# Optimization experiments

Hardware: AMD Instinct MI355X
Metric: run time of the kernel (lower is better)

## Reference

```python
import jax, jax.numpy as jnp
import numpy as np

D_MODEL = 1024
NHEAD = 16
HEAD_DIM = D_MODEL // NHEAD
SF_THRESHOLD = 4.0
SF_LEVELS = 8
SF_STEP = SF_THRESHOLD / SF_LEVELS  # 0.5
EPS = 1e-6


def sfn(x):
    # Scale-and-Fire neuron: quantize activations to multiples of SF_STEP,
    # clipped to +/- num_levels, with straight-through estimator.
    q = jnp.clip(jnp.round(x / SF_STEP), -SF_LEVELS, SF_LEVELS) * SF_STEP
    return x + jax.lax.stop_gradient(q - x)


def qk_norm(x, g):
    # RMS-normalize over the head_dim (last axis) with learnable gain g [Dh].
    rms = jnp.sqrt(jnp.mean(x * x, axis=-1, keepdims=True) + EPS)
    return (x / rms) * g


def setup_inputs() -> dict:
    key = jax.random.key(0)
    ks = jax.random.split(key, 10)
    B, L, D = 2, 2048, D_MODEL
    s = 1.0 / np.sqrt(D)
    return {
        "x": jax.random.normal(ks[0], (B, L, D), dtype=jnp.float32),
        "Wq": jax.random.normal(ks[1], (D, D), dtype=jnp.float32) * s,
        "bq": jnp.zeros((D,), dtype=jnp.float32),
        "Wk": jax.random.normal(ks[2], (D, D), dtype=jnp.float32) * s,
        "bk": jnp.zeros((D,), dtype=jnp.float32),
        "Wv": jax.random.normal(ks[3], (D, D), dtype=jnp.float32) * s,
        "bv": jnp.zeros((D,), dtype=jnp.float32),
        "Wo": jax.random.normal(ks[4], (D, D), dtype=jnp.float32) * s,
        "bo": jnp.zeros((D,), dtype=jnp.float32),
        "gq": jnp.ones((HEAD_DIM,), dtype=jnp.float32),
        "gk": jnp.ones((HEAD_DIM,), dtype=jnp.float32),
    }


def reference(x, Wq, bq, Wk, bk, Wv, bv, Wo, bo, gq, gk):
    B, L, D = x.shape
    H, Dh = NHEAD, HEAD_DIM
    scale = Dh ** (-0.5)

    q = sfn(x @ Wq.T + bq)
    k = sfn(x @ Wk.T + bk)
    v = sfn(x @ Wv.T + bv)

    # [B, L, H, Dh] -> [B, H, L, Dh]
    q = q.reshape(B, L, H, Dh).transpose(0, 2, 1, 3)
    k = k.reshape(B, L, H, Dh).transpose(0, 2, 1, 3)
    v = v.reshape(B, L, H, Dh).transpose(0, 2, 1, 3)

    q = qk_norm(q, gq)
    k = qk_norm(k, gk)

    scores = jnp.einsum('bhqd,bhkd->bhqk', q, k) * scale
    probs = jax.nn.softmax(scores, axis=-1)  # dropout is identity (eval)
    out = jnp.einsum('bhqk,bhkd->bhqd', probs, v)
    out = out.transpose(0, 2, 1, 3).reshape(B, L, D)
    return out @ Wo.T + bo
```

## Files before the change

kernel.cpp:

```cpp
#include <hip/hip_runtime.h>
#include <math.h>


typedef __bf16 bf16;
typedef bf16 bf16x4 __attribute__((ext_vector_type(4)));
typedef bf16 bf16x8 __attribute__((ext_vector_type(8)));
typedef float f32x4 __attribute__((ext_vector_type(4)));

#define LOG2E 1.4426950408889634f
#define MFMA16 __builtin_amdgcn_mfma_f32_16x16x32_bf16
#define S_WAITV(N) asm volatile("s_waitcnt vmcnt(" #N ")" ::: "memory")

__device__ __forceinline__ void bar() {
  asm volatile("" ::: "memory");
  __builtin_amdgcn_s_barrier();
  asm volatile("" ::: "memory");
}

__device__ __forceinline__ float sfn_f(float x) {
  return fminf(fmaxf(rintf(x + x), -8.0f), 8.0f) * 0.5f;
}

__device__ __forceinline__ void gload16(const bf16* g, bf16* l) {
  __builtin_amdgcn_global_load_lds((const __attribute__((address_space(1))) void*)g,
                                   (__attribute__((address_space(3))) void*)l, 16, 0, 0);
}


__global__ __launch_bounds__(256) void prep_x_kernel(const float* __restrict__ x,
                                                     bf16* __restrict__ ax) {
  int idx = blockIdx.x * 256 + threadIdx.x;
  int m  = idx >> 8;
  int kc = (idx & 255) << 2;
  const float4 v = *(const float4*)(x + (size_t)m * 1024 + kc);
  bf16 h0 = (bf16)v.x, h1 = (bf16)v.y, h2 = (bf16)v.z, h3 = (bf16)v.w;
  bf16 l0 = (bf16)(v.x - (float)h0), l1 = (bf16)(v.y - (float)h1),
       l2 = (bf16)(v.z - (float)h2), l3 = (bf16)(v.w - (float)h3);
  bf16x4 hv = {h0, h1, h2, h3};
  bf16x4 lv = {l0, l1, l2, l3};
  bf16* p = ax + (size_t)m * 3072 + kc;
  *(bf16x4*)(p)        = hv;
  *(bf16x4*)(p + 1024) = lv;
  *(bf16x4*)(p + 2048) = hv;
}

__global__ __launch_bounds__(256) void prep_w_kernel(const float* __restrict__ Wq,
                                                     const float* __restrict__ Wk,
                                                     const float* __restrict__ Wv,
                                                     bf16* __restrict__ wc) {
  int idx = blockIdx.x * 256 + threadIdx.x;
  int mat = idx >> 18;
  int r   = idx & 262143;
  int n   = r >> 8;
  int kc  = (r & 255) << 2;
  const float* W = (mat == 0) ? Wq : ((mat == 1) ? Wk : Wv);
  const float4 v = *(const float4*)(W + (size_t)n * 1024 + kc);
  bf16 h0 = (bf16)v.x, h1 = (bf16)v.y, h2 = (bf16)v.z, h3 = (bf16)v.w;
  bf16 l0 = (bf16)(v.x - (float)h0), l1 = (bf16)(v.y - (float)h1),
       l2 = (bf16)(v.z - (float)h2), l3 = (bf16)(v.w - (float)h3);
  bf16x4 hv = {h0, h1, h2, h3};
  bf16x4 lv = {l0, l1, l2, l3};
  bf16* p = wc + (size_t)(mat * 1024 + n) * 3072 + kc;
  *(bf16x4*)(p)        = hv;
  *(bf16x4*)(p + 1024) = hv;
  *(bf16x4*)(p + 2048) = lv;
}

__global__ __launch_bounds__(256) void prep_wo_kernel(const float* __restrict__ Wo,
                                                      bf16* __restrict__ wob) {
  int idx = blockIdx.x * 256 + threadIdx.x;
  const float4 v = *(const float4*)(Wo + (size_t)idx * 4);
  bf16x4 hv = {(bf16)v.x, (bf16)v.y, (bf16)v.z, (bf16)v.w};
  *(bf16x4*)(wob + (size_t)idx * 4) = hv;
}


__global__ __launch_bounds__(512, 2) void gemm_qkv_kernel(
    const bf16* __restrict__ A, const bf16* __restrict__ Bm,
    const float* __restrict__ b0, const float* __restrict__ b1,
    const float* __restrict__ b2, const float* __restrict__ g0,
    const float* __restrict__ g1, bf16* __restrict__ qn, bf16* __restrict__ kn,
    bf16* __restrict__ vt) {
  constexpr int K = 3072, NT = 48;
  __shared__ bf16 lds[2][28672];
  const int tid  = threadIdx.x;
  const int wave = tid >> 6;
  const int lane = tid & 63;
  const int lm   = lane & 15;
  const int kg   = lane >> 4;
  const int lid     = blockIdx.x;
  const int logical = ((lid & 7) << 5) | (lid >> 3);
  const int m0 = (logical >> 4) << 8;
  const int n0 = (logical & 15) * 192;

  auto stageA = [&](int buf, int half, int kt) {
#pragma unroll
    for (int j = 0; j < 2; ++j) {
      const int c    = j * 512 + tid;
      const int row  = c >> 3;
      const int col8 = (c & 7) ^ (row & 7);
      gload16(A + (size_t)(m0 + half * 128 + row) * K + kt + col8 * 8,
              &lds[buf][half * 8192 + c * 8]);
    }
  };
  auto stageB = [&](int buf, int ch, int kt) {
    const int row  = tid >> 3;
    const int col8 = (tid & 7) ^ (row & 7);
    gload16(Bm + (size_t)(n0 + ch * 64 + row) * K + kt + col8 * 8,
            &lds[buf][16384 + ch * 4096 + tid * 8]);
  };

  const int sw    = lm & 7;
  const int arow  = (wave << 5) + lm;
  auto rdA = [&](int buf, int r, int kk) -> bf16x8 {
    const int row = arow + 16 * r;
    return *(const bf16x8*)&lds[buf][(row >> 7) * 8192 + (row & 127) * 64 +
                                     (((kk << 2) + kg) ^ sw) * 8];
  };
  auto rdB = [&](int buf, int c, int kk) -> bf16x8 {
    const int col = 16 * c + lm;
    return *(const bf16x8*)&lds[buf][16384 + (col >> 6) * 4096 + (col & 63) * 64 +
                                     (((kk << 2) + kg) ^ sw) * 8];
  };

  f32x4 acc[2][12] = {};

  stageA(0, 0, 0); stageA(0, 1, 0);
  stageB(0, 0, 0); stageB(0, 1, 0); stageB(0, 2, 0);
  stageA(1, 0, 64); stageA(1, 1, 64);
  S_WAITV(4);
  bar();

  for (int t = 0; t < NT; ++t) {
    const int cur = t & 1, nxt = cur ^ 1;
    const int kt1 = (t + 1) << 6, kt2 = (t + 2) << 6;
    bf16x8 a[2][2], bv[6];
#pragma unroll
    for (int r = 0; r < 2; ++r)
#pragma unroll
      for (int kk = 0; kk < 2; ++kk)
        a[r][kk] = rdA(cur, r, kk);
#pragma unroll
    for (int c = 0; c < 6; ++c) bv[c] = rdB(cur, c, 0);
    if (t + 1 < NT) stageB(nxt, 0, kt1);
    bar();
    __builtin_amdgcn_s_setprio(1);
#pragma unroll
    for (int r = 0; r < 2; ++r)
#pragma unroll
      for (int c = 0; c < 6; ++c)
        acc[r][c] = MFMA16(a[r][0], bv[c], acc[r][c], 0, 0, 0);
    __builtin_amdgcn_s_setprio(0);
    bar();
    bf16x8 bw[6];
#pragma unroll
    for (int c = 0; c < 6; ++c) bw[c] = rdB(cur, c + 6, 0);
    if (t + 1 < NT) { stageB(nxt, 1, kt1); stageB(nxt, 2, kt1); }
    bar();
    __builtin_amdgcn_s_setprio(1);
#pragma unroll
    for (int r = 0; r < 2; ++r)
#pragma unroll
      for (int c = 0; c < 6; ++c)
        acc[r][c + 6] = MFMA16(a[r][0], bw[c], acc[r][c + 6], 0, 0, 0);
    __builtin_amdgcn_s_setprio(0);
    bar();
    bf16x8 bx[6];
#pragma unroll
    for (int c = 0; c < 6; ++c) bx[c] = rdB(cur, c, 1);
    bar();
    __builtin_amdgcn_s_setprio(1);
#pragma unroll
    for (int r = 0; r < 2; ++r)
#pragma unroll
      for (int c = 0; c < 6; ++c)
        acc[r][c] = MFMA16(a[r][1], bx[c], acc[r][c], 0, 0, 0);
    __builtin_amdgcn_s_setprio(0);
    bar();
    bf16x8 by[6];
#pragma unroll
    for (int c = 0; c < 6; ++c) by[c] = rdB(cur, c + 6, 1);
    if (t + 2 < NT) {
      stageA(cur, 0, kt2); stageA(cur, 1, kt2);
      S_WAITV(4);
    } else {
      S_WAITV(0);
    }
    bar();
    __builtin_amdgcn_s_setprio(1);
#pragma unroll
    for (int r = 0; r < 2; ++r)
#pragma unroll
      for (int c = 0; c < 6; ++c)
        acc[r][c + 6] = MFMA16(a[r][1], by[c], acc[r][c + 6], 0, 0, 0);
    __builtin_amdgcn_s_setprio(0);
    bar();
  }

#pragma unroll
  for (int h = 0; h < 3; ++h) {
    const int gcol = n0 + (h << 6);
    const int mat  = gcol >> 10;
    const int cb   = gcol & 1023;
    const int hh   = cb >> 6;
    const float* bias = (mat == 0) ? b0 : ((mat == 1) ? b1 : b2);
    float bvals[4];
#pragma unroll
    for (int j = 0; j < 4; ++j) bvals[j] = bias[cb + 16 * j + lm];

    if (mat < 2) {
      const float* gain = (mat == 0) ? g0 : g1;
      bf16* dst = (mat == 0) ? qn : kn;
      float gv[4];
#pragma unroll
      for (int j = 0; j < 4; ++j) gv[j] = gain[16 * j + lm];
#pragma unroll
      for (int r = 0; r < 2; ++r) {
        float y[4][4];
        float ss[4] = {0.f, 0.f, 0.f, 0.f};
#pragma unroll
        for (int j = 0; j < 4; ++j)
#pragma unroll
          for (int g = 0; g < 4; ++g) {
            float tq = sfn_f(acc[r][4 * h + j][g] + bvals[j]);
            y[j][g] = tq;
            ss[g] += tq * tq;
          }
#pragma unroll
        for (int g = 0; g < 4; ++g) {
          float s = ss[g];
          s += __shfl_xor(s, 1);
          s += __shfl_xor(s, 2);
          s += __shfl_xor(s, 4);
          s += __shfl_xor(s, 8);
          ss[g] = 1.0f / sqrtf(s * (1.0f / 64.0f) + 1e-6f);
        }
        const int mbase = m0 + (wave << 5) + 16 * r + 4 * kg;
        const int bb = mbase >> 11;
        const int ll = mbase & 2047;
#pragma unroll
        for (int g = 0; g < 4; ++g) {
          bf16* rowp = dst + ((size_t)(bb * 16 + hh) * 2048 + (ll + g)) * 64;
#pragma unroll
          for (int j = 0; j < 4; ++j)
            rowp[16 * j + lm] = (bf16)(y[j][g] * ss[g] * gv[j]);
        }
      }
    } else {
#pragma unroll
      for (int r = 0; r < 2; ++r) {
        const int mbase = m0 + (wave << 5) + 16 * r + 4 * kg;
        const int bb = mbase >> 11;
        const int ll = mbase & 2047;
#pragma unroll
        for (int j = 0; j < 4; ++j) {
          bf16x4 pk;
#pragma unroll
          for (int g = 0; g < 4; ++g)
            pk[g] = (bf16)sfn_f(acc[r][4 * h + j][g] + bvals[j]);
          *(bf16x4*)(vt + ((size_t)(bb * 16 + hh) * 64 + 16 * j + lm) * 2048 + ll) = pk;
        }
      }
    }
  }
}


__global__ __launch_bounds__(256, 3) void gemm_o_kernel(
    const bf16* __restrict__ A, const bf16* __restrict__ Bm, int K,
    const float* __restrict__ b0, float* __restrict__ outf) {
  __shared__ bf16 sA[128 * 32];
  __shared__ bf16 sB[128 * 32];
  const int tid  = threadIdx.x;
  const int wave = tid >> 6;
  const int lane = tid & 63;
  const int lm   = lane & 15;
  const int kg   = lane >> 4;
  const int nbx = gridDim.x;
  const int lid = blockIdx.x + nbx * blockIdx.y;
  const int cpx = (nbx << 5) >> 3;
  const int logical = (lid & 7) * cpx + (lid >> 3);
  const int m0 = (logical / nbx) << 7;
  const int n0 = (logical % nbx) << 7;
  const int wm = (wave >> 1) << 6;
  const int wn = (wave & 1) << 6;

  f32x4 acc[4][4] = {};

  for (int kt = 0; kt < K; kt += 32) {
    __syncthreads();
#pragma unroll
    for (int j = 0; j < 2; ++j) {
      const int i   = wave * 128 + j * 64 + lane;
      const int row = i >> 2;
      const int kc  = (i & 3) << 3;
      gload16(A  + (size_t)(m0 + row) * K + kt + kc, sA + i * 8);
      gload16(Bm + (size_t)(n0 + row) * K + kt + kc, sB + i * 8);
    }
    __syncthreads();
    bf16x8 af[4], bfv[4];
#pragma unroll
    for (int r = 0; r < 4; ++r)
      af[r] = *(const bf16x8*)(sA + (wm + 16 * r + lm) * 32 + kg * 8);
#pragma unroll
    for (int c = 0; c < 4; ++c)
      bfv[c] = *(const bf16x8*)(sB + (wn + 16 * c + lm) * 32 + kg * 8);
#pragma unroll
    for (int r = 0; r < 4; ++r)
#pragma unroll
      for (int c = 0; c < 4; ++c)
        acc[r][c] = MFMA16(af[r], bfv[c], acc[r][c], 0, 0, 0);
  }

  float bvals[4];
#pragma unroll
  for (int c = 0; c < 4; ++c) bvals[c] = b0[n0 + wn + 16 * c + lm];
#pragma unroll
  for (int r = 0; r < 4; ++r) {
    const int mr = m0 + wm + 16 * r + 4 * kg;
#pragma unroll
    for (int c = 0; c < 4; ++c) {
      const int nc = n0 + wn + 16 * c + lm;
#pragma unroll
      for (int g = 0; g < 4; ++g)
        outf[(size_t)(mr + g) * 1024 + nc] = acc[r][c][g] + bvals[c];
    }
  }
}


__global__ __launch_bounds__(256, 3) void attn_kernel(const bf16* __restrict__ qn,
                                                      const bf16* __restrict__ kn,
                                                      const bf16* __restrict__ vt,
                                                      bf16* __restrict__ ao) {
  __shared__ bf16 sK[3][64 * 64];
  __shared__ bf16 sV[2][64 * 64];
  __shared__ bf16 sP[4][16 * 72];
  const int tid  = threadIdx.x;
  const int wave = tid >> 6;
  const int lane = tid & 63;
  const int lm   = lane & 15;
  const int kg   = lane >> 4;
  const int lid     = blockIdx.x + (blockIdx.y << 4);
  const int logical = ((lid & 7) << 6) | (lid >> 3);
  const int qblk    = logical & 15;
  const int bh      = logical >> 4;
  const int q0      = (qblk << 7) + (wave << 5);
  const bf16* qb = qn + (size_t)bh * 2048 * 64;
  const bf16* kb = kn + (size_t)bh * 2048 * 64;
  const bf16* vb = vt + (size_t)bh * 64 * 2048;

  const float C1 = 0.125f * LOG2E;
  const float C2 = -8.0f * LOG2E;

  const int srow7 = lane >> 3;
  const int scl   = (lane & 7) ^ srow7;
  auto stageK = [&](int buf, int kt) {
#pragma unroll
    for (int j = 0; j < 2; ++j) {
      const int ci  = wave * 2 + j;
      const int row = ci * 8 + srow7;
      gload16(kb + (size_t)(kt + row) * 64 + scl * 8, &sK[buf][ci * 512]);
    }
  };
  auto stageV = [&](int buf, int kt) {
#pragma unroll
    for (int j = 0; j < 2; ++j) {
      const int ci  = wave * 2 + j;
      const int row = ci * 8 + srow7;
      gload16(vb + (size_t)row * 2048 + kt + scl * 8, &sV[buf][ci * 512]);
    }
  };

  bf16x8 qf[2][2];
#pragma unroll
  for (int c = 0; c < 2; ++c)
#pragma unroll
    for (int dh = 0; dh < 2; ++dh)
      qf[c][dh] = *(const bf16x8*)(qb + (size_t)(q0 + 16 * c + lm) * 64 + dh * 32 + kg * 8);

  f32x4 o[4][2] = {};
  float lrun[2] = {0.f, 0.f};
  bf16x8 pb[2][2];
  const int a7 = lm & 7;

  stageV(0, 0);
  stageK(0, 0);
  stageK(1, 64);
  S_WAITV(0);
  bar();
  {
    bf16x8 ka[4][2];
#pragma unroll
    for (int rb = 0; rb < 4; ++rb)
#pragma unroll
      for (int dh = 0; dh < 2; ++dh)
        ka[rb][dh] = *(const bf16x8*)(&sK[0][(16 * rb + lm) * 64 + ((dh * 4 + kg) ^ a7) * 8]);
    f32x4 s[4][2] = {};
#pragma unroll
    for (int rb = 0; rb < 4; ++rb)
#pragma unroll
      for (int c = 0; c < 2; ++c)
#pragma unroll
        for (int dh = 0; dh < 2; ++dh)
          s[rb][c] = MFMA16(ka[rb][dh], qf[c][dh], s[rb][c], 0, 0, 0);
#pragma unroll
    for (int c = 0; c < 2; ++c) {
#pragma unroll
      for (int rb = 0; rb < 4; ++rb) {
        bf16x4 pk;
#pragma unroll
        for (int g = 0; g < 4; ++g) {
          float p = __builtin_amdgcn_exp2f(fmaf(s[rb][c][g], C1, C2));
          lrun[c] += p;
          pk[g] = (bf16)p;
        }
        *(bf16x4*)(&sP[wave][lm * 72 + 16 * rb + 4 * kg]) = pk;
      }
      asm volatile("s_waitcnt lgkmcnt(0)" ::: "memory");
#pragma unroll
      for (int kh = 0; kh < 2; ++kh)
        pb[c][kh] = *(const bf16x8*)(&sP[wave][lm * 72 + kh * 32 + kg * 8]);
    }
  }
  stageK(2, 128);
  bar();

  for (int t = 0; t < 32; ++t) {
    const int vcur = t & 1;
    if (t + 1 < 32) stageV((t + 1) & 1, (t + 1) << 6);
    if (t + 3 < 32) stageK((t + 3) % 3, (t + 3) << 6);

    f32x4 s[4][2];
    if (t + 1 < 32) {
      const bf16* kbuf = sK[(t + 1) % 3];
      bf16x8 ka[4][2];
#pragma unroll
      for (int rb = 0; rb < 4; ++rb)
#pragma unroll
        for (int dh = 0; dh < 2; ++dh)
          ka[rb][dh] = *(const bf16x8*)(&kbuf[(16 * rb + lm) * 64 + ((dh * 4 + kg) ^ a7) * 8]);
#pragma unroll
      for (int rb = 0; rb < 4; ++rb)
#pragma unroll
        for (int c = 0; c < 2; ++c)
          s[rb][c] = f32x4{0.f, 0.f, 0.f, 0.f};
      __builtin_amdgcn_s_setprio(1);
#pragma unroll
      for (int rb = 0; rb < 4; ++rb)
#pragma unroll
        for (int c = 0; c < 2; ++c)
#pragma unroll
          for (int dh = 0; dh < 2; ++dh)
            s[rb][c] = MFMA16(ka[rb][dh], qf[c][dh], s[rb][c], 0, 0, 0);
      __builtin_amdgcn_s_setprio(0);
    }

    {
      bf16x8 va[4][2];
#pragma unroll
      for (int rbd = 0; rbd < 4; ++rbd)
#pragma unroll
        for (int kh = 0; kh < 2; ++kh)
          va[rbd][kh] = *(const bf16x8*)(&sV[vcur][(16 * rbd + lm) * 64 + ((kh * 4 + kg) ^ a7) * 8]);
      __builtin_amdgcn_s_setprio(1);
#pragma unroll
      for (int rbd = 0; rbd < 4; ++rbd)
#pragma unroll
        for (int c = 0; c < 2; ++c)
#pragma unroll
          for (int kh = 0; kh < 2; ++kh)
            o[rbd][c] = MFMA16(va[rbd][kh], pb[c][kh], o[rbd][c], 0, 0, 0);
      __builtin_amdgcn_s_setprio(0);
    }

    if (t + 1 < 32) {
#pragma unroll
      for (int c = 0; c < 2; ++c) {
#pragma unroll
        for (int rb = 0; rb < 4; ++rb) {
          bf16x4 pk;
#pragma unroll
          for (int g = 0; g < 4; ++g) {
            float p = __builtin_amdgcn_exp2f(fmaf(s[rb][c][g], C1, C2));
            lrun[c] += p;
            pk[g] = (bf16)p;
          }
          *(bf16x4*)(&sP[wave][lm * 72 + 16 * rb + 4 * kg]) = pk;
        }
        asm volatile("s_waitcnt lgkmcnt(0)" ::: "memory");
#pragma unroll
        for (int kh = 0; kh < 2; ++kh)
          pb[c][kh] = *(const bf16x8*)(&sP[wave][lm * 72 + kh * 32 + kg * 8]);
      }
    }

    if (t + 3 < 32) { S_WAITV(2); } else { S_WAITV(0); }
    bar();
  }

  const int bb = bh >> 4;
  const int hh = bh & 15;
#pragma unroll
  for (int c = 0; c < 2; ++c) {
    float l = lrun[c];
    l += __shfl_xor(l, 16);
    l += __shfl_xor(l, 32);
    const float inv = 1.0f / l;
    const int q = q0 + 16 * c + lm;
    bf16* rowp = ao + (size_t)(bb * 2048 + q) * 1024 + hh * 64;
#pragma unroll
    for (int rbd = 0; rbd < 4; ++rbd) {
      bf16x4 pk;
#pragma unroll
      for (int g = 0; g < 4; ++g)
        pk[g] = (bf16)(o[rbd][c][g] * inv);
      *(bf16x4*)(rowp + 16 * rbd + 4 * kg) = pk;
    }
  }
}


extern "C" void kernel_launch(void* const* d_in, const int* in_sizes, int n_in,
                              void* d_out, int out_size, void* d_ws, size_t ws_size,
                              hipStream_t stream) {
  const float* x  = (const float*)d_in[0];
  const float* Wq = (const float*)d_in[1];
  const float* bq = (const float*)d_in[2];
  const float* Wk = (const float*)d_in[3];
  const float* bk = (const float*)d_in[4];
  const float* Wv = (const float*)d_in[5];
  const float* bv = (const float*)d_in[6];
  const float* Wo = (const float*)d_in[7];
  const float* bo = (const float*)d_in[8];
  const float* gq = (const float*)d_in[9];
  const float* gk = (const float*)d_in[10];
  float* out = (float*)d_out;

  char* ws = (char*)d_ws;
  bf16* ax   = (bf16*)(ws);
  bf16* wc   = (bf16*)(ws + 25165824);
  bf16* wob  = (bf16*)(ws + 44040192);
  bf16* qn   = (bf16*)(ws + 46137344);
  bf16* kn   = (bf16*)(ws + 54525952);
  bf16* vt   = (bf16*)(ws + 62914560);
  bf16* attn = (bf16*)(ws + 71303168);

  prep_x_kernel<<<dim3(4096), dim3(256), 0, stream>>>(x, ax);
  prep_w_kernel<<<dim3(3072), dim3(256), 0, stream>>>(Wq, Wk, Wv, wc);
  prep_wo_kernel<<<dim3(1024), dim3(256), 0, stream>>>(Wo, wob);

  gemm_qkv_kernel<<<dim3(256), dim3(512), 0, stream>>>(
      ax, wc, bq, bk, bv, gq, gk, qn, kn, vt);

  attn_kernel<<<dim3(16, 32), dim3(256), 0, stream>>>(qn, kn, vt, attn);

  gemm_o_kernel<<<dim3(8, 32), dim3(256), 0, stream>>>(
      attn, wob, 1024, bo, out);
}
```

Measured before the change: 247.6 us.

## Rewrite attention with 32x32x16 MFMA and register-resident P via permlane32 swap

The attention kernel moves from 16x16x32 to 32x32x16 bf16 MFMA tiles, computing S^T per 32-key slice and feeding the exponentiated probabilities straight into the PV MFMA. It uses v_permlane32_swap instead of a round trip through shared memory for P. The software pipeline is simplified from a triple-buffered K with a skewed S/PV schedule to plain double buffering of K and V, with launch bounds lowered to 2 blocks per CU. This removes the LDS traffic and waits for P, but gives up the overlap between QK and PV across iterations and may reduce occupancy.

```diff
diff --git a/kernel.cpp b/kernel.cpp
--- a/kernel.cpp
+++ b/kernel.cpp
@@ -6,9 +6,13 @@
 typedef bf16 bf16x4 __attribute__((ext_vector_type(4)));
 typedef bf16 bf16x8 __attribute__((ext_vector_type(8)));
 typedef float f32x4 __attribute__((ext_vector_type(4)));
+typedef float f32x16 __attribute__((ext_vector_type(16)));
+typedef unsigned int u32;
+typedef u32 u32x4 __attribute__((ext_vector_type(4)));
 
 #define LOG2E 1.4426950408889634f
 #define MFMA16 __builtin_amdgcn_mfma_f32_16x16x32_bf16
+#define MFMA32 __builtin_amdgcn_mfma_f32_32x32x16_bf16
 #define S_WAITV(N) asm volatile("s_waitcnt vmcnt(" #N ")" ::: "memory")
 
 __device__ __forceinline__ void bar() {
@@ -24,6 +28,12 @@
 __device__ __forceinline__ void gload16(const bf16* g, bf16* l) {
   __builtin_amdgcn_global_load_lds((const __attribute__((address_space(1))) void*)g,
                                    (__attribute__((address_space(3))) void*)l, 16, 0, 0);
+}
+
+__device__ __forceinline__ u32 pkbf16(float a, float b) {
+  unsigned short ua = __builtin_bit_cast(unsigned short, (bf16)a);
+  unsigned short ub = __builtin_bit_cast(unsigned short, (bf16)b);
+  return (u32)ua | ((u32)ub << 16);
 }
 
 
@@ -329,18 +339,17 @@
 }
 
 
-__global__ __launch_bounds__(256, 3) void attn_kernel(const bf16* __restrict__ qn,
+__global__ __launch_bounds__(256, 2) void attn_kernel(const bf16* __restrict__ qn,
                                                       const bf16* __restrict__ kn,
                                                       const bf16* __restrict__ vt,
                                                       bf16* __restrict__ ao) {
-  __shared__ bf16 sK[3][64 * 64];
+  __shared__ bf16 sK[2][64 * 64];
   __shared__ bf16 sV[2][64 * 64];
-  __shared__ bf16 sP[4][16 * 72];
   const int tid  = threadIdx.x;
   const int wave = tid >> 6;
   const int lane = tid & 63;
-  const int lm   = lane & 15;
-  const int kg   = lane >> 4;
+  const int l31  = lane & 31;
+  const int hi   = lane >> 5;
   const int lid     = blockIdx.x + (blockIdx.y << 4);
   const int logical = ((lid & 7) << 6) | (lid >> 3);
   const int qblk    = logical & 15;
@@ -372,152 +381,89 @@
     }
   };
 
-  bf16x8 qf[2][2];
-#pragma unroll
-  for (int c = 0; c < 2; ++c)
-#pragma unroll
-    for (int dh = 0; dh < 2; ++dh)
-      qf[c][dh] = *(const bf16x8*)(qb + (size_t)(q0 + 16 * c + lm) * 64 + dh * 32 + kg * 8);
-
-  f32x4 o[4][2] = {};
-  float lrun[2] = {0.f, 0.f};
-  bf16x8 pb[2][2];
-  const int a7 = lm & 7;
-
+  bf16x8 qf[4];
+#pragma unroll
+  for (int j = 0; j < 4; ++j)
+    qf[j] = *(const bf16x8*)(qb + (size_t)(q0 + l31) * 64 + j * 16 + hi * 8);
+
+  f32x16 o[2] = {};
+  float lrun = 0.f;
+
+  stageK(0, 0);
   stageV(0, 0);
-  stageK(0, 0);
-  stageK(1, 64);
   S_WAITV(0);
   bar();
-  {
-    bf16x8 ka[4][2];
-#pragma unroll
-    for (int rb = 0; rb < 4; ++rb)
-#pragma unroll
-      for (int dh = 0; dh < 2; ++dh)
-        ka[rb][dh] = *(const bf16x8*)(&sK[0][(16 * rb + lm) * 64 + ((dh * 4 + kg) ^ a7) * 8]);
-    f32x4 s[4][2] = {};
-#pragma unroll
-    for (int rb = 0; rb < 4; ++rb)
-#pragma unroll
-      for (int c = 0; c < 2; ++c)
-#pragma unroll
-        for (int dh = 0; dh < 2; ++dh)
-          s[rb][c] = MFMA16(ka[rb][dh], qf[c][dh], s[rb][c], 0, 0, 0);
-#pragma unroll
-    for (int c = 0; c < 2; ++c) {
-#pragma unroll
-      for (int rb = 0; rb < 4; ++rb) {
-        bf16x4 pk;
-#pragma unroll
-        for (int g = 0; g < 4; ++g) {
-          float p = __builtin_amdgcn_exp2f(fmaf(s[rb][c][g], C1, C2));
-          lrun[c] += p;
-          pk[g] = (bf16)p;
-        }
-        *(bf16x4*)(&sP[wave][lm * 72 + 16 * rb + 4 * kg]) = pk;
+
+  for (int t = 0; t < 32; ++t) {
+    const int cur = t & 1;
+    if (t < 31) { stageK(cur ^ 1, (t + 1) << 6); stageV(cur ^ 1, (t + 1) << 6); }
+
+#pragma unroll
+    for (int ks = 0; ks < 2; ++ks) {
+      const int krow = ks * 32 + l31;
+      const int ksw  = krow & 7;
+      bf16x8 kf[4];
+#pragma unroll
+      for (int j = 0; j < 4; ++j)
+        kf[j] = *(const bf16x8*)(&sK[cur][krow * 64 + ((2 * j + hi) ^ ksw) * 8]);
+
+      f32x16 s = {0.f, 0.f, 0.f, 0.f, 0.f, 0.f, 0.f, 0.f,
+                  0.f, 0.f, 0.f, 0.f, 0.f, 0.f, 0.f, 0.f};
+      __builtin_amdgcn_s_setprio(1);
+#pragma unroll
+      for (int j = 0; j < 4; ++j)
+        s = MFMA32(kf[j], qf[j], s, 0, 0, 0);
+      __builtin_amdgcn_s_setprio(0);
+
+      float p[16];
+#pragma unroll
+      for (int r = 0; r < 16; ++r) {
+        p[r] = __builtin_amdgcn_exp2f(fmaf(s[r], C1, C2));
+        lrun += p[r];
       }
-      asm volatile("s_waitcnt lgkmcnt(0)" ::: "memory");
-#pragma unroll
-      for (int kh = 0; kh < 2; ++kh)
-        pb[c][kh] = *(const bf16x8*)(&sP[wave][lm * 72 + kh * 32 + kg * 8]);
-    }
+      u32 w0 = pkbf16(p[0], p[1]),  w1 = pkbf16(p[2], p[3]);
+      u32 w2 = pkbf16(p[4], p[5]),  w3 = pkbf16(p[6], p[7]);
+      u32 w4 = pkbf16(p[8], p[9]),  w5 = pkbf16(p[10], p[11]);
+      u32 w6 = pkbf16(p[12], p[13]), w7 = pkbf16(p[14], p[15]);
+      asm volatile("v_permlane32_swap_b32 %0, %1" : "+v"(w0), "+v"(w2));
+      asm volatile("v_permlane32_swap_b32 %0, %1" : "+v"(w1), "+v"(w3));
+      asm volatile("v_permlane32_swap_b32 %0, %1" : "+v"(w4), "+v"(w6));
+      asm volatile("v_permlane32_swap_b32 %0, %1" : "+v"(w5), "+v"(w7));
+      const bf16x8 pb0 = __builtin_bit_cast(bf16x8, (u32x4){w0, w1, w2, w3});
+      const bf16x8 pb1 = __builtin_bit_cast(bf16x8, (u32x4){w4, w5, w6, w7});
+
+#pragma unroll
+      for (int rb = 0; rb < 2; ++rb) {
+        const int vrow = rb * 32 + l31;
+        const int vsw  = vrow & 7;
+        const bf16x8 vf0 = *(const bf16x8*)(&sV[cur][vrow * 64 + ((4 * ks + hi) ^ vsw) * 8]);
+        const bf16x8 vf1 = *(const bf16x8*)(&sV[cur][vrow * 64 + ((4 * ks + 2 + hi) ^ vsw) * 8]);
+        __builtin_amdgcn_s_setprio(1);
+        o[rb] = MFMA32(vf0, pb0, o[rb], 0, 0, 0);
+        o[rb] = MFMA32(vf1, pb1, o[rb], 0, 0, 0);
+        __builtin_amdgcn_s_setprio(0);
+      }
+    }
+
+    S_WAITV(0);
+    bar();
   }
-  stageK(2, 128);
-  bar();
-
-  for (int t = 0; t < 32; ++t) {
-    const int vcur = t & 1;
-    if (t + 1 < 32) stageV((t + 1) & 1, (t + 1) << 6);
-    if (t + 3 < 32) stageK((t + 3) % 3, (t + 3) << 6);
-
-    f32x4 s[4][2];
-    if (t + 1 < 32) {
-      const bf16* kbuf = sK[(t + 1) % 3];
-      bf16x8 ka[4][2];
-#pragma unroll
-      for (int rb = 0; rb < 4; ++rb)
-#pragma unroll
-        for (int dh = 0; dh < 2; ++dh)
-          ka[rb][dh] = *(const bf16x8*)(&kbuf[(16 * rb + lm) * 64 + ((dh * 4 + kg) ^ a7) * 8]);
-#pragma unroll
-      for (int rb = 0; rb < 4; ++rb)
-#pragma unroll
-        for (int c = 0; c < 2; ++c)
-          s[rb][c] = f32x4{0.f, 0.f, 0.f, 0.f};
-      __builtin_amdgcn_s_setprio(1);
-#pragma unroll
-      for (int rb = 0; rb < 4; ++rb)
-#pragma unroll
-        for (int c = 0; c < 2; ++c)
-#pragma unroll
-          for (int dh = 0; dh < 2; ++dh)
-            s[rb][c] = MFMA16(ka[rb][dh], qf[c][dh], s[rb][c], 0, 0, 0);
-      __builtin_amdgcn_s_setprio(0);
-    }
-
-    {
-      bf16x8 va[4][2];
-#pragma unroll
-      for (int rbd = 0; rbd < 4; ++rbd)
-#pragma unroll
-        for (int kh = 0; kh < 2; ++kh)
-          va[rbd][kh] = *(const bf16x8*)(&sV[vcur][(16 * rbd + lm) * 64 + ((kh * 4 + kg) ^ a7) * 8]);
-      __builtin_amdgcn_s_setprio(1);
-#pragma unroll
-      for (int rbd = 0; rbd < 4; ++rbd)
-#pragma unroll
-        for (int c = 0; c < 2; ++c)
-#pragma unroll
-          for (int kh = 0; kh < 2; ++kh)
-            o[rbd][c] = MFMA16(va[rbd][kh], pb[c][kh], o[rbd][c], 0, 0, 0);
-      __builtin_amdgcn_s_setprio(0);
-    }
-
-    if (t + 1 < 32) {
-#pragma unroll
-      for (int c = 0; c < 2; ++c) {
-#pragma unroll
-        for (int rb = 0; rb < 4; ++rb) {
-          bf16x4 pk;
-#pragma unroll
-          for (int g = 0; g < 4; ++g) {
-            float p = __builtin_amdgcn_exp2f(fmaf(s[rb][c][g], C1, C2));
-            lrun[c] += p;
-            pk[g] = (bf16)p;
-          }
-          *(bf16x4*)(&sP[wave][lm * 72 + 16 * rb + 4 * kg]) = pk;
-        }
-        asm volatile("s_waitcnt lgkmcnt(0)" ::: "memory");
-#pragma unroll
-        for (int kh = 0; kh < 2; ++kh)
-          pb[c][kh] = *(const bf16x8*)(&sP[wave][lm * 72 + kh * 32 + kg * 8]);
-      }
-    }
-
-    if (t + 3 < 32) { S_WAITV(2); } else { S_WAITV(0); }
-    bar();
-  }
-
+
+  lrun += __shfl_xor(lrun, 32);
+  const float inv = 1.0f / lrun;
   const int bb = bh >> 4;
   const int hh = bh & 15;
-#pragma unroll
-  for (int c = 0; c < 2; ++c) {
-    float l = lrun[c];
-    l += __shfl_xor(l, 16);
-    l += __shfl_xor(l, 32);
-    const float inv = 1.0f / l;
-    const int q = q0 + 16 * c + lm;
-    bf16* rowp = ao + (size_t)(bb * 2048 + q) * 1024 + hh * 64;
-#pragma unroll
-    for (int rbd = 0; rbd < 4; ++rbd) {
+  bf16* rowp = ao + (size_t)(bb * 2048 + q0 + l31) * 1024 + hh * 64;
+#pragma unroll
+  for (int rb = 0; rb < 2; ++rb)
+#pragma unroll
+    for (int r4 = 0; r4 < 4; ++r4) {
       bf16x4 pk;
 #pragma unroll
       for (int g = 0; g < 4; ++g)
-        pk[g] = (bf16)(o[rbd][c][g] * inv);
-      *(bf16x4*)(rowp + 16 * rbd + 4 * kg) = pk;
-    }
-  }
+        pk[g] = (bf16)(o[rb][r4 * 4 + g] * inv);
+      *(bf16x4*)(rowp + rb * 32 + r4 * 8 + hi * 4) = pk;
+    }
 }
 
 
```

Measured after the change: 252.3 us. About the same (+1.9%).
